# Performance work log

Measured on AMD Instinct MI355X. Metric: run time of the kernel, lower is better.

The kernel has to match this reference:

```python
import jax, jax.numpy as jnp
import numpy as np

N_NODES = 50000


def _gcn_conv(x, src, dst, W, b, n):
    # linear transform first (PyG GCNConv: self.lin has no bias; bias added after aggregation)
    h = x @ W  # [N, out]
    # symmetric normalization with self-loops already appended in (src, dst)
    ones = jnp.ones(src.shape[0], dtype=h.dtype)
    deg = jax.ops.segment_sum(ones, dst, num_segments=n)  # in-degree incl. self-loop
    dinv = jnp.where(deg > 0, jax.lax.rsqrt(deg), 0.0)
    norm = dinv[src] * dinv[dst]  # [E+N]
    msg = h[src] * norm[:, None]  # gather + scale
    out = jax.ops.segment_sum(msg, dst, num_segments=n)  # scatter-add
    return out + b


def setup_inputs() -> dict:
    key = jax.random.key(0)
    ks = jax.random.split(key, 8)
    f_in, h1, h2, n_cls = 256, 128, 128, 40
    E = 800000
    x = jax.random.normal(ks[0], (N_NODES, f_in), dtype=jnp.float32)
    edge_index = jax.random.randint(ks[1], (2, E), 0, N_NODES, dtype=jnp.int64)
    def glorot(k, fi, fo):
        s = jnp.sqrt(6.0 / (fi + fo)).astype(jnp.float32)
        return jax.random.uniform(k, (fi, fo), jnp.float32, -s, s)
    return {
        "x": x,
        "edge_index": edge_index,
        "W1": glorot(ks[2], f_in, h1), "b1": jnp.zeros((h1,), jnp.float32),
        "W2": glorot(ks[3], h1, h2), "b2": jnp.zeros((h2,), jnp.float32),
        "W3": glorot(ks[4], h2, n_cls), "b3": jnp.zeros((n_cls,), jnp.float32),
    }


def reference(x, edge_index, W1, b1, W2, b2, W3, b3):
    n = x.shape[0]
    loop = jnp.arange(n, dtype=edge_index.dtype)
    src = jnp.concatenate([edge_index[0], loop])  # add self-loops (fill_value=1.0)
    dst = jnp.concatenate([edge_index[1], loop])
    h = _gcn_conv(x, src, dst, W1, b1, n)
    h = jax.nn.relu(h)  # dropout is identity in eval mode
    h = _gcn_conv(h, src, dst, W2, b2, n)
    h = jax.nn.relu(h)
    h = _gcn_conv(h, src, dst, W3, b3, n)
    return jax.nn.log_softmax(h, axis=1)
```

## Files before the change

### kernel.cpp

```cpp
#include <hip/hip_runtime.h>
#include <cstdint>
#include <cstddef>
#include <cmath>


typedef __attribute__((ext_vector_type(8))) short short8;
typedef __attribute__((ext_vector_type(4))) float f32x4;

constexpr int EPB = 4096;

__device__ __forceinline__ ushort f2bf(float f) {
  union { float f; uint32_t u; } x; x.f = f;
  uint32_t r = x.u + 0x7fffu + ((x.u >> 16) & 1u);
  return (ushort)(r >> 16);
}
__device__ __forceinline__ float bf2f(ushort u) {
  union { uint32_t u; float f; } x; x.u = ((uint32_t)u) << 16;
  return x.f;
}

__global__ __launch_bounds__(256) void bucket_hist_kernel(const int* __restrict__ dst,
                                                          int* __restrict__ bucket_count,
                                                          int E) {
  __shared__ int h[256];
  const int t  = threadIdx.x;
  const int e0 = blockIdx.x * EPB;
  const int myE = min(EPB, E - e0);
  h[t] = 0;
  __syncthreads();
  for (int i = t; i < myE; i += 256) atomicAdd(&h[dst[e0 + i] >> 8], 1);
  __syncthreads();
  if (h[t]) atomicAdd(&bucket_count[t], h[t]);
}

__global__ __launch_bounds__(256) void bucket_scan_kernel(const int* __restrict__ bucket_count,
                                                          int* __restrict__ bucket_offs,
                                                          int* __restrict__ bucket_cursor,
                                                          int* __restrict__ offs,
                                                          int nbuck, int n) {
  __shared__ int s[256];
  const int t = threadIdx.x;
  const int c = (t < nbuck) ? bucket_count[t] : 0;
  s[t] = c;
  __syncthreads();
  for (int off = 1; off < 256; off <<= 1) {
    int v = (t >= off) ? s[t - off] : 0;
    __syncthreads();
    s[t] += v;
    __syncthreads();
  }
  if (t < nbuck) {
    bucket_offs[t]   = s[t] - c;
    bucket_cursor[t] = s[t] - c;
  }
  if (t == 255) {
    bucket_offs[nbuck] = s[255];
    offs[n] = s[255];
  }
}

__global__ __launch_bounds__(256) void bucket_scatter_kernel(const int* __restrict__ src,
                                                             const int* __restrict__ dst,
                                                             int* __restrict__ bucket_cursor,
                                                             int2* __restrict__ staged,
                                                             int E, int nbuck) {
  __shared__ int hist[256], s[256], lstart[256], cbase[256], lcur[256];
  __shared__ int2 stage[EPB];
  const int t  = threadIdx.x;
  const int e0 = blockIdx.x * EPB;
  const int myE = min(EPB, E - e0);
  hist[t] = 0;
  __syncthreads();
  for (int i = t; i < myE; i += 256) atomicAdd(&hist[dst[e0 + i] >> 8], 1);
  __syncthreads();
  const int c = hist[t];
  s[t] = c;
  __syncthreads();
  for (int off = 1; off < 256; off <<= 1) {
    int v = (t >= off) ? s[t - off] : 0;
    __syncthreads();
    s[t] += v;
    __syncthreads();
  }
  lstart[t] = s[t] - c;
  lcur[t]   = s[t] - c;
  cbase[t]  = (c > 0 && t < nbuck) ? atomicAdd(&bucket_cursor[t], c) : 0;
  __syncthreads();
  for (int i = t; i < myE; i += 256) {
    const int sv = src[e0 + i], dv = dst[e0 + i];
    const int slot = atomicAdd(&lcur[dv >> 8], 1);
    stage[slot] = make_int2(sv, dv);
  }
  __syncthreads();
  for (int i = t; i < myE; i += 256) {
    const int2 sd = stage[i];
    const int b = sd.y >> 8;
    staged[cbase[b] + (i - lstart[b])] = sd;
  }
}

__global__ __launch_bounds__(256) void bucket_csr_kernel(const int2* __restrict__ staged,
                                                         const int* __restrict__ bucket_offs,
                                                         int* __restrict__ offs,
                                                         float* __restrict__ dinv, int n) {
  __shared__ int cnt[256], s[256];
  const int t = threadIdx.x, b = blockIdx.x;
  cnt[t] = 0;
  __syncthreads();
  const int ebeg = bucket_offs[b], eend = bucket_offs[b + 1];
  for (int i = ebeg + t; i < eend; i += 256) atomicAdd(&cnt[staged[i].y & 255], 1);
  __syncthreads();
  const int c = cnt[t];
  s[t] = c;
  __syncthreads();
  for (int off = 1; off < 256; off <<= 1) {
    int v = (t >= off) ? s[t - off] : 0;
    __syncthreads();
    s[t] += v;
    __syncthreads();
  }
  const int node = (b << 8) + t;
  if (node < n) {
    offs[node] = ebeg + s[t] - c;
    dinv[node] = rsqrtf((float)(c + 1));
  }
}

__global__ __launch_bounds__(256) void bucket_fill_kernel(const int2* __restrict__ staged,
                                                          const int* __restrict__ bucket_offs,
                                                          const float* __restrict__ dinv,
                                                          int2* __restrict__ epair, int n) {
  __shared__ int cnt[256], s[256], cur[256];
  const int t = threadIdx.x, b = blockIdx.x;
  cnt[t] = 0;
  __syncthreads();
  const int ebeg = bucket_offs[b], eend = bucket_offs[b + 1];
  for (int i = ebeg + t; i < eend; i += 256) atomicAdd(&cnt[staged[i].y & 255], 1);
  __syncthreads();
  const int c = cnt[t];
  s[t] = c;
  __syncthreads();
  for (int off = 1; off < 256; off <<= 1) {
    int v = (t >= off) ? s[t - off] : 0;
    __syncthreads();
    s[t] += v;
    __syncthreads();
  }
  cur[t] = ebeg + s[t] - c;
  __syncthreads();
  for (int i = ebeg + t; i < eend; i += 256) {
    const int2 sd = staged[i];
    const int pos = atomicAdd(&cur[sd.y & 255], 1);
    epair[pos] = make_int2(sd.x, __float_as_int(dinv[sd.x] * dinv[sd.y]));
  }
}

__global__ __launch_bounds__(256) void pack_w_kernel(const float* __restrict__ W,
                                                     ushort* __restrict__ Wp,
                                                     int K, int N, int NF) {
  const int idx  = blockIdx.x * blockDim.x + threadIdx.x;
  const int lane = idx & 63;
  const int nf   = (idx >> 6) % NF;
  const int g    = idx / (64 * NF);
  if (g * 32 >= K) return;
  const int n  = nf * 16 + (lane & 15);
  const int kb = g * 32 + (lane >> 4) * 8;
  ushort v[8];
#pragma unroll
  for (int j = 0; j < 8; ++j) {
    const float f = (n < N) ? W[(size_t)(kb + j) * N + n] : 0.f;
    v[j] = f2bf(f);
  }
  *(short8*)&Wp[((size_t)(g * NF + nf) * 64 + lane) * 8] = *(short8*)v;
}

template <int NF, bool AF32>
__global__ __launch_bounds__(256) void mfma_gemm_kernel(const void* __restrict__ Av,
                                                        const ushort* __restrict__ Wp,
                                                        ushort* __restrict__ C,
                                                        int M, int N, int K) {
  __shared__ ushort Atile[64 * 64];
  const int tid  = threadIdx.x;
  const int lane = tid & 63;
  const int wave = tid >> 6;
  const int brow = blockIdx.x * 64;

  f32x4 acc[NF];
#pragma unroll
  for (int nf = 0; nf < NF; ++nf) acc[nf] = (f32x4){0.f, 0.f, 0.f, 0.f};

  const int arow = wave * 16 + (lane & 15);
  const int ahi  = lane >> 4;
  const int row0 = tid >> 3;
  const int kc0  = tid & 7;

  for (int k0 = 0; k0 < K; k0 += 64) {
    if (k0) __syncthreads();
#pragma unroll
    for (int c = 0; c < 2; ++c) {
      const int row = row0 + c * 32;
      const int gr  = brow + row;
      short8 v = (short8){0, 0, 0, 0, 0, 0, 0, 0};
      if (gr < M) {
        if constexpr (AF32) {
          const float* A = (const float*)Av + (size_t)gr * K + k0 + kc0 * 8;
          const float4 f0 = *(const float4*)A;
          const float4 f1 = *(const float4*)(A + 4);
          v[0] = (short)f2bf(f0.x); v[1] = (short)f2bf(f0.y);
          v[2] = (short)f2bf(f0.z); v[3] = (short)f2bf(f0.w);
          v[4] = (short)f2bf(f1.x); v[5] = (short)f2bf(f1.y);
          v[6] = (short)f2bf(f1.z); v[7] = (short)f2bf(f1.w);
        } else {
          v = *(const short8*)((const ushort*)Av + (size_t)gr * K + k0 + kc0 * 8);
        }
      }
      *(short8*)&Atile[row * 64 + ((kc0 ^ (row & 7)) * 8)] = v;
    }
    __syncthreads();

    const int gbase = (k0 >> 5) * NF;
#pragma unroll
    for (int kk = 0; kk < 2; ++kk) {
      const int kc = kk * 4 + ahi;
      const short8 a =
          *(const short8*)&Atile[arow * 64 + ((kc ^ (arow & 7)) * 8)];
      const ushort* wp = Wp + ((size_t)(gbase + kk * NF) * 64 + lane) * 8;
#pragma unroll
      for (int nf = 0; nf < NF; ++nf) {
        const short8 b = *(const short8*)(wp + (size_t)nf * 64 * 8);
        acc[nf] = __builtin_amdgcn_mfma_f32_16x16x32_bf16(a, b, acc[nf], 0, 0, 0);
      }
    }
  }

  const int crow0 = brow + wave * 16 + (lane >> 4) * 4;
  const int ccol  = lane & 15;
#pragma unroll
  for (int nf = 0; nf < NF; ++nf) {
    const int col = nf * 16 + ccol;
    if (col < N) {
#pragma unroll
      for (int r = 0; r < 4; ++r) {
        const int row = crow0 + r;
        if (row < M) C[(size_t)row * N + col] = f2bf(acc[nf][r]);
      }
    }
  }
}

__global__ __launch_bounds__(256) void mfma_gemm_lsm_kernel(const ushort* __restrict__ A,
                                                            const ushort* __restrict__ Wp,
                                                            const float* __restrict__ bias,
                                                            float* __restrict__ out,
                                                            int M, int N, int K) {
  constexpr int NF = 3;
  __shared__ ushort Atile[64 * 64];
  const int tid  = threadIdx.x;
  const int lane = tid & 63;
  const int wave = tid >> 6;
  const int brow = blockIdx.x * 64;

  f32x4 acc[NF];
#pragma unroll
  for (int nf = 0; nf < NF; ++nf) acc[nf] = (f32x4){0.f, 0.f, 0.f, 0.f};

  const int arow = wave * 16 + (lane & 15);
  const int ahi  = lane >> 4;
  const int row0 = tid >> 3;
  const int kc0  = tid & 7;

  for (int k0 = 0; k0 < K; k0 += 64) {
    if (k0) __syncthreads();
#pragma unroll
    for (int c = 0; c < 2; ++c) {
      const int row = row0 + c * 32;
      const int gr  = brow + row;
      short8 v = (short8){0, 0, 0, 0, 0, 0, 0, 0};
      if (gr < M)
        v = *(const short8*)&A[(size_t)gr * K + k0 + kc0 * 8];
      *(short8*)&Atile[row * 64 + ((kc0 ^ (row & 7)) * 8)] = v;
    }
    __syncthreads();

    const int gbase = (k0 >> 5) * NF;
#pragma unroll
    for (int kk = 0; kk < 2; ++kk) {
      const int kc = kk * 4 + ahi;
      const short8 a =
          *(const short8*)&Atile[arow * 64 + ((kc ^ (arow & 7)) * 8)];
      const ushort* wp = Wp + ((size_t)(gbase + kk * NF) * 64 + lane) * 8;
#pragma unroll
      for (int nf = 0; nf < NF; ++nf) {
        const short8 b = *(const short8*)(wp + (size_t)nf * 64 * 8);
        acc[nf] = __builtin_amdgcn_mfma_f32_16x16x32_bf16(a, b, acc[nf], 0, 0, 0);
      }
    }
  }

  const int ccol  = lane & 15;
  const int crow0 = brow + wave * 16 + (lane >> 4) * 4;
  float bv[NF];
#pragma unroll
  for (int nf = 0; nf < NF; ++nf) {
    const int col = nf * 16 + ccol;
    bv[nf] = (col < N) ? bias[col] : 0.f;
  }
  const bool v2ok = (32 + ccol) < N;
#pragma unroll
  for (int r = 0; r < 4; ++r) {
    const float v0 = acc[0][r] + bv[0];
    const float v1 = acc[1][r] + bv[1];
    const float v2 = acc[2][r] + bv[2];
    float m = fmaxf(v0, v1);
    if (v2ok) m = fmaxf(m, v2);
#pragma unroll
    for (int o = 8; o >= 1; o >>= 1) m = fmaxf(m, __shfl_xor(m, o, 64));
    float s = expf(v0 - m) + expf(v1 - m) + (v2ok ? expf(v2 - m) : 0.f);
#pragma unroll
    for (int o = 8; o >= 1; o >>= 1) s += __shfl_xor(s, o, 64);
    const float mls = m + logf(s);
    const int row = crow0 + r;
    if (row < M) {
      out[(size_t)row * N + ccol]      = v0 - mls;
      out[(size_t)row * N + 16 + ccol] = v1 - mls;
      if (v2ok) out[(size_t)row * N + 32 + ccol] = v2 - mls;
    }
  }
}

template <bool BIAS_RELU>
__global__ __launch_bounds__(256) void agg4_kernel(const ushort* __restrict__ h,
                                                   const int* __restrict__ offsets,
                                                   const int2* __restrict__ epair,
                                                   const float* __restrict__ dinv,
                                                   const float* __restrict__ bias,
                                                   ushort* __restrict__ out, int n) {
  const int wave = threadIdx.x >> 6;
  const int lane = threadIdx.x & 63;
  const int node = blockIdx.x * 4 + wave;
  if (node >= n) return;
  const int eg = lane >> 4;
  const int f0 = (lane & 15) * 8;

  float acc[8];
#pragma unroll
  for (int j = 0; j < 8; ++j) acc[j] = 0.f;

  const int start = offsets[node];
  const int end   = offsets[node + 1];
  for (int eb = start; eb < end; eb += 8) {
    const int e0 = eb + eg;
    const int e1 = e0 + 4;
    if (e0 < end) {
      const int2  sw0 = epair[e0];
      const float w0  = __int_as_float(sw0.y);
      const short8 hv0 = *(const short8*)&h[(size_t)sw0.x * 128 + f0];
      if (e1 < end) {
        const int2  sw1 = epair[e1];
        const float w1  = __int_as_float(sw1.y);
        const short8 hv1 = *(const short8*)&h[(size_t)sw1.x * 128 + f0];
#pragma unroll
        for (int j = 0; j < 8; ++j) {
          acc[j] = fmaf(bf2f((ushort)hv0[j]), w0, acc[j]);
          acc[j] = fmaf(bf2f((ushort)hv1[j]), w1, acc[j]);
        }
      } else {
#pragma unroll
        for (int j = 0; j < 8; ++j) acc[j] = fmaf(bf2f((ushort)hv0[j]), w0, acc[j]);
      }
    }
  }
#pragma unroll
  for (int j = 0; j < 8; ++j) {
    acc[j] += __shfl_xor(acc[j], 16, 64);
    acc[j] += __shfl_xor(acc[j], 32, 64);
  }
  if (eg == 0) {
    const float di  = dinv[node];
    const float di2 = di * di;
    const short8 hs = *(const short8*)&h[(size_t)node * 128 + f0];
    ushort o[8];
#pragma unroll
    for (int j = 0; j < 8; ++j) {
      float a = fmaf(bf2f((ushort)hs[j]), di2, acc[j]);
      if (BIAS_RELU) a = fmaxf(a + bias[f0 + j], 0.f);
      o[j] = f2bf(a);
    }
    *(short8*)&out[(size_t)node * 128 + f0] = *(short8*)o;
  }
}

extern "C" void kernel_launch(void* const* d_in, const int* in_sizes, int n_in,
                              void* d_out, int out_size, void* d_ws, size_t ws_size,
                              hipStream_t stream) {
  const float* x  = (const float*)d_in[0];
  const int*   ei = (const int*)d_in[1];
  const float* W1 = (const float*)d_in[2];
  const float* b1 = (const float*)d_in[3];
  const float* W2 = (const float*)d_in[4];
  const float* b2 = (const float*)d_in[5];
  const float* W3 = (const float*)d_in[6];
  const float* b3 = (const float*)d_in[7];

  const int h1   = in_sizes[3];
  const int h2   = in_sizes[5];
  const int ncls = in_sizes[7];
  const int fin  = in_sizes[2] / h1;
  const int n    = in_sizes[0] / fin;
  const int E    = in_sizes[1] / 2;

  const int* src = ei;
  const int* dst = ei + E;

  char* p = (char*)d_ws;
  auto alloc = [&](size_t bytes) {
    char* r = p;
    p += (bytes + 255) & ~size_t(255);
    return r;
  };
  float*  dinv   = (float*)alloc((size_t)n * 4);
  int*    offs   = (int*)alloc((size_t)(n + 1) * 4);
  int*    bcount = (int*)alloc(256 * 4);
  int*    boffs  = (int*)alloc(257 * 4);
  int*    bcur   = (int*)alloc(256 * 4);
  int2*   staged = (int2*)alloc((size_t)E * 8);
  int2*   epair  = (int2*)alloc((size_t)E * 8);
  ushort* hf     = (ushort*)alloc((size_t)n * h1 * 2);
  ushort* hb     = (ushort*)alloc((size_t)n * h1 * 2);
  ushort* Wp1    = (ushort*)alloc((size_t)(fin / 32) * 8 * 64 * 8 * 2);
  ushort* Wp2    = (ushort*)alloc((size_t)(h1 / 32) * 8 * 64 * 8 * 2);
  ushort* Wp3    = (ushort*)alloc((size_t)(h2 / 32) * 3 * 64 * 8 * 2);

  const int nbuck = (n + 255) >> 8;
  const int ebw   = (E + EPB - 1) / EPB;

  hipMemsetAsync(bcount, 0, 256 * 4, stream);
  bucket_hist_kernel<<<ebw, 256, 0, stream>>>(dst, bcount, E);
  bucket_scan_kernel<<<1, 256, 0, stream>>>(bcount, boffs, bcur, offs, nbuck, n);
  bucket_scatter_kernel<<<ebw, 256, 0, stream>>>(src, dst, bcur, staged, E, nbuck);
  bucket_csr_kernel<<<nbuck, 256, 0, stream>>>(staged, boffs, offs, dinv, n);
  bucket_fill_kernel<<<nbuck, 256, 0, stream>>>(staged, boffs, dinv, epair, n);

  {
    int t1 = (fin / 32) * 8 * 64;
    int t2 = (h1 / 32) * 8 * 64;
    int t3 = (h2 / 32) * 3 * 64;
    pack_w_kernel<<<(t1 + 255) / 256, 256, 0, stream>>>(W1, Wp1, fin, h1, 8);
    pack_w_kernel<<<(t2 + 255) / 256, 256, 0, stream>>>(W2, Wp2, h1, h2, 8);
    pack_w_kernel<<<(t3 + 255) / 256, 256, 0, stream>>>(W3, Wp3, h2, ncls, 3);
  }

  const int gblocks = (n + 63) / 64;
  const int ablocks = (n + 3) / 4;

  mfma_gemm_kernel<8, true><<<gblocks, 256, 0, stream>>>(x, Wp1, hf, n, h1, fin);
  agg4_kernel<true><<<ablocks, 256, 0, stream>>>(hf, offs, epair, dinv, b1, hb, n);
  mfma_gemm_kernel<8, false><<<gblocks, 256, 0, stream>>>(hb, Wp2, hf, n, h2, h1);
  agg4_kernel<true><<<ablocks, 256, 0, stream>>>(hf, offs, epair, dinv, b2, hb, n);
  agg4_kernel<false><<<ablocks, 256, 0, stream>>>(hb, offs, epair, dinv, nullptr, hf, n);
  mfma_gemm_lsm_kernel<<<gblocks, 256, 0, stream>>>(hf, Wp3, b3, (float*)d_out,
                                                    n, ncls, h2);
}
```

Baseline: 216.1 us.

## Fuse neighbor aggregation into following MFMA GEMM to skip intermediate round trip

Adds an agg_gemm kernel that aggregates 64 node rows into shared memory and then runs the MFMA GEMM on that tile directly. It replaces the agg+GEMM pair for layer 2 and the agg+GEMM+log-softmax tail for layer 3, so the aggregated activations no longer go to global memory and are never re-read. The cost is that each wave now aggregates 16 nodes one after another inside a 64-row block. This lowers the parallelism of the gather phase and may hurt latency hiding for the irregular memory access.

Measured after the change: 262.0 us. 21.3% more time.

```diff
diff --git a/kernel.cpp b/kernel.cpp
--- a/kernel.cpp
+++ b/kernel.cpp
@@ -248,46 +248,95 @@
   }
 }
 
-__global__ __launch_bounds__(256) void mfma_gemm_lsm_kernel(const ushort* __restrict__ A,
-                                                            const ushort* __restrict__ Wp,
-                                                            const float* __restrict__ bias,
-                                                            float* __restrict__ out,
-                                                            int M, int N, int K) {
-  constexpr int NF = 3;
-  __shared__ ushort Atile[64 * 64];
+template <int NF, bool BIAS_RELU_AGG, bool LSM>
+__global__ __launch_bounds__(256) void agg_gemm_kernel(
+    const ushort* __restrict__ h, const int* __restrict__ offsets,
+    const int2* __restrict__ epair, const float* __restrict__ dinv,
+    const float* __restrict__ bias_agg, const ushort* __restrict__ Wp,
+    const float* __restrict__ bias_out, void* __restrict__ Cv, int M, int N) {
+  __shared__ ushort Atile[2][64 * 64];
   const int tid  = threadIdx.x;
   const int lane = tid & 63;
   const int wave = tid >> 6;
   const int brow = blockIdx.x * 64;
 
+  const int eg    = lane >> 4;
+  const int l15   = lane & 15;
+  const int f0    = l15 * 8;
+  const int ktile = l15 >> 3;
+  const int kca   = l15 & 7;
+
+  for (int i = 0; i < 16; ++i) {
+    const int row  = wave * 16 + i;
+    const int node = brow + row;
+    float a8[8];
+#pragma unroll
+    for (int j = 0; j < 8; ++j) a8[j] = 0.f;
+    if (node < M) {
+      const int start = offsets[node];
+      const int end   = offsets[node + 1];
+      for (int eb = start; eb < end; eb += 8) {
+        const int e0 = eb + eg;
+        const int e1 = e0 + 4;
+        if (e0 < end) {
+          const int2  sw0 = epair[e0];
+          const float w0  = __int_as_float(sw0.y);
+          const short8 hv0 = *(const short8*)&h[(size_t)sw0.x * 128 + f0];
+          if (e1 < end) {
+            const int2  sw1 = epair[e1];
+            const float w1  = __int_as_float(sw1.y);
+            const short8 hv1 = *(const short8*)&h[(size_t)sw1.x * 128 + f0];
+#pragma unroll
+            for (int j = 0; j < 8; ++j) {
+              a8[j] = fmaf(bf2f((ushort)hv0[j]), w0, a8[j]);
+              a8[j] = fmaf(bf2f((ushort)hv1[j]), w1, a8[j]);
+            }
+          } else {
+#pragma unroll
+            for (int j = 0; j < 8; ++j) a8[j] = fmaf(bf2f((ushort)hv0[j]), w0, a8[j]);
+          }
+        }
+      }
+#pragma unroll
+      for (int j = 0; j < 8; ++j) {
+        a8[j] += __shfl_xor(a8[j], 16, 64);
+        a8[j] += __shfl_xor(a8[j], 32, 64);
+      }
+    }
+    if (eg == 0) {
+      ushort o[8];
+      if (node < M) {
+        const float di  = dinv[node];
+        const float di2 = di * di;
+        const short8 hs = *(const short8*)&h[(size_t)node * 128 + f0];
+#pragma unroll
+        for (int j = 0; j < 8; ++j) {
+          float a = fmaf(bf2f((ushort)hs[j]), di2, a8[j]);
+          if (BIAS_RELU_AGG) a = fmaxf(a + bias_agg[f0 + j], 0.f);
+          o[j] = f2bf(a);
+        }
+      } else {
+#pragma unroll
+        for (int j = 0; j < 8; ++j) o[j] = 0;
+      }
+      *(short8*)&Atile[ktile][row * 64 + ((kca ^ (row & 7)) << 3)] = *(short8*)o;
+    }
+  }
+  __syncthreads();
+
   f32x4 acc[NF];
 #pragma unroll
   for (int nf = 0; nf < NF; ++nf) acc[nf] = (f32x4){0.f, 0.f, 0.f, 0.f};
-
   const int arow = wave * 16 + (lane & 15);
   const int ahi  = lane >> 4;
-  const int row0 = tid >> 3;
-  const int kc0  = tid & 7;
-
-  for (int k0 = 0; k0 < K; k0 += 64) {
-    if (k0) __syncthreads();
-#pragma unroll
-    for (int c = 0; c < 2; ++c) {
-      const int row = row0 + c * 32;
-      const int gr  = brow + row;
-      short8 v = (short8){0, 0, 0, 0, 0, 0, 0, 0};
-      if (gr < M)
-        v = *(const short8*)&A[(size_t)gr * K + k0 + kc0 * 8];
-      *(short8*)&Atile[row * 64 + ((kc0 ^ (row & 7)) * 8)] = v;
-    }
-    __syncthreads();
-
-    const int gbase = (k0 >> 5) * NF;
+#pragma unroll
+  for (int kt = 0; kt < 2; ++kt) {
+    const int gbase = kt * 2 * NF;
 #pragma unroll
     for (int kk = 0; kk < 2; ++kk) {
       const int kc = kk * 4 + ahi;
       const short8 a =
-          *(const short8*)&Atile[arow * 64 + ((kc ^ (arow & 7)) * 8)];
+          *(const short8*)&Atile[kt][arow * 64 + ((kc ^ (arow & 7)) * 8)];
       const ushort* wp = Wp + ((size_t)(gbase + kk * NF) * 64 + lane) * 8;
 #pragma unroll
       for (int nf = 0; nf < NF; ++nf) {
@@ -299,31 +348,47 @@
 
   const int ccol  = lane & 15;
   const int crow0 = brow + wave * 16 + (lane >> 4) * 4;
-  float bv[NF];
-#pragma unroll
-  for (int nf = 0; nf < NF; ++nf) {
-    const int col = nf * 16 + ccol;
-    bv[nf] = (col < N) ? bias[col] : 0.f;
-  }
-  const bool v2ok = (32 + ccol) < N;
-#pragma unroll
-  for (int r = 0; r < 4; ++r) {
-    const float v0 = acc[0][r] + bv[0];
-    const float v1 = acc[1][r] + bv[1];
-    const float v2 = acc[2][r] + bv[2];
-    float m = fmaxf(v0, v1);
-    if (v2ok) m = fmaxf(m, v2);
-#pragma unroll
-    for (int o = 8; o >= 1; o >>= 1) m = fmaxf(m, __shfl_xor(m, o, 64));
-    float s = expf(v0 - m) + expf(v1 - m) + (v2ok ? expf(v2 - m) : 0.f);
-#pragma unroll
-    for (int o = 8; o >= 1; o >>= 1) s += __shfl_xor(s, o, 64);
-    const float mls = m + logf(s);
-    const int row = crow0 + r;
-    if (row < M) {
-      out[(size_t)row * N + ccol]      = v0 - mls;
-      out[(size_t)row * N + 16 + ccol] = v1 - mls;
-      if (v2ok) out[(size_t)row * N + 32 + ccol] = v2 - mls;
+  if constexpr (!LSM) {
+    ushort* C = (ushort*)Cv;
+#pragma unroll
+    for (int nf = 0; nf < NF; ++nf) {
+      const int col = nf * 16 + ccol;
+      if (col < N) {
+#pragma unroll
+        for (int r = 0; r < 4; ++r) {
+          const int row = crow0 + r;
+          if (row < M) C[(size_t)row * N + col] = f2bf(acc[nf][r]);
+        }
+      }
+    }
+  } else {
+    float* out = (float*)Cv;
+    float bv[NF];
+#pragma unroll
+    for (int nf = 0; nf < NF; ++nf) {
+      const int col = nf * 16 + ccol;
+      bv[nf] = (col < N) ? bias_out[col] : 0.f;
+    }
+    const bool v2ok = (32 + ccol) < N;
+#pragma unroll
+    for (int r = 0; r < 4; ++r) {
+      const float v0 = acc[0][r] + bv[0];
+      const float v1 = acc[1][r] + bv[1];
+      const float v2 = acc[2][r] + bv[2];
+      float m = fmaxf(v0, v1);
+      if (v2ok) m = fmaxf(m, v2);
+#pragma unroll
+      for (int o = 8; o >= 1; o >>= 1) m = fmaxf(m, __shfl_xor(m, o, 64));
+      float s = expf(v0 - m) + expf(v1 - m) + (v2ok ? expf(v2 - m) : 0.f);
+#pragma unroll
+      for (int o = 8; o >= 1; o >>= 1) s += __shfl_xor(s, o, 64);
+      const float mls = m + logf(s);
+      const int row = crow0 + r;
+      if (row < M) {
+        out[(size_t)row * N + ccol]      = v0 - mls;
+        out[(size_t)row * N + 16 + ccol] = v1 - mls;
+        if (v2ok) out[(size_t)row * N + 32 + ccol] = v2 - mls;
+      }
     }
   }
 }
@@ -426,7 +491,8 @@
   int2*   staged = (int2*)alloc((size_t)E * 8);
   int2*   epair  = (int2*)alloc((size_t)E * 8);
   ushort* hf     = (ushort*)alloc((size_t)n * h1 * 2);
-  ushort* hb     = (ushort*)alloc((size_t)n * h1 * 2);
+  ushort* hg     = (ushort*)alloc((size_t)n * h1 * 2);
+  ushort* hb     = hf;
   ushort* Wp1    = (ushort*)alloc((size_t)(fin / 32) * 8 * 64 * 8 * 2);
   ushort* Wp2    = (ushort*)alloc((size_t)(h1 / 32) * 8 * 64 * 8 * 2);
   ushort* Wp3    = (ushort*)alloc((size_t)(h2 / 32) * 3 * 64 * 8 * 2);
@@ -454,10 +520,9 @@
   const int ablocks = (n + 3) / 4;
 
   mfma_gemm_kernel<8, true><<<gblocks, 256, 0, stream>>>(x, Wp1, hf, n, h1, fin);
-  agg4_kernel<true><<<ablocks, 256, 0, stream>>>(hf, offs, epair, dinv, b1, hb, n);
-  mfma_gemm_kernel<8, false><<<gblocks, 256, 0, stream>>>(hb, Wp2, hf, n, h2, h1);
-  agg4_kernel<true><<<ablocks, 256, 0, stream>>>(hf, offs, epair, dinv, b2, hb, n);
-  agg4_kernel<false><<<ablocks, 256, 0, stream>>>(hb, offs, epair, dinv, nullptr, hf, n);
-  mfma_gemm_lsm_kernel<<<gblocks, 256, 0, stream>>>(hf, Wp3, b3, (float*)d_out,
-                                                    n, ncls, h2);
-}
+  agg_gemm_kernel<8, true, false><<<gblocks, 256, 0, stream>>>(
+      hf, offs, epair, dinv, b1, Wp2, nullptr, hg, n, h2);
+  agg4_kernel<true><<<ablocks, 256, 0, stream>>>(hg, offs, epair, dinv, b2, hb, n);
+  agg_gemm_kernel<3, false, true><<<gblocks, 256, 0, stream>>>(
+      hb, offs, epair, dinv, nullptr, Wp3, b3, d_out, n, ncls);
+}
```
